# Performance work log

Hardware: AMD Instinct MI355X
Metric: run time of the kernel (lower is better)

The kernel has to match this reference:

```python
import jax, jax.numpy as jnp
import numpy as np
import math

EMBD_SIZE = 1024
OUT_SIZE = 1024
B, N = 8, 2048

def setup_inputs() -> dict:
    key = jax.random.key(0)
    k1, k2, k3 = jax.random.split(key, 3)
    embd = jax.random.normal(k1, (B, N, EMBD_SIZE), dtype=jnp.float32)
    # nn.Linear(embd_size, out_size): weight [out, in], bias [out]
    bound = 1.0 / math.sqrt(EMBD_SIZE)
    W = jax.random.uniform(k2, (OUT_SIZE, EMBD_SIZE), dtype=jnp.float32, minval=-bound, maxval=bound)
    b = jax.random.uniform(k3, (OUT_SIZE,), dtype=jnp.float32, minval=-bound, maxval=bound)
    return {"embd": embd, "W": W, "b": b}

def reference(embd, W, b):
    # c = Linear(embd): [B, N, out_size]
    c = jnp.einsum('bne,oe->bno', embd, W) + b
    # scores = c @ c^T / sqrt(embd_size), softmax over last dim
    score = jnp.einsum('bno,bmo->bnm', c, c) / jnp.sqrt(jnp.float32(EMBD_SIZE))
    score = jax.nn.softmax(score, axis=-1)
    # output = score @ c : [B, N, out_size]
    return jnp.einsum('bnm,bmo->bno', score, c)
```

## Files before the change

### kernel.cpp

```cpp
#include <hip/hip_runtime.h>

typedef unsigned short u16;
typedef unsigned int u32;
typedef __attribute__((ext_vector_type(8))) short short8;
typedef __attribute__((ext_vector_type(4))) float f32x4;

__device__ inline u16 f2bf(float f) {
  u32 x = __float_as_uint(f);
  x += 0x7fff + ((x >> 16) & 1);
  return (u16)(x >> 16);
}
__device__ inline float bf2f(u16 h) {
  return __uint_as_float(((u32)h) << 16);
}
__device__ inline void gload16(const void* g, void* l) {
  __builtin_amdgcn_global_load_lds((const __attribute__((address_space(1))) u32*)g,
                                   (__attribute__((address_space(3))) u32*)l, 16, 0, 0);
}

__device__ inline int sg(int r) {
  return ((r >> 3) & 7) ^ (((r >> 2) & 1) << 2) ^ (((r >> 3) & 1) << 1);
}
__device__ inline int stile_off(int rl, int cl) {
  return rl * 128 + (((cl >> 3) ^ sg(rl)) << 3) + (cl & 7);
}

__global__ void cast_all(const float* __restrict__ embd, const float* __restrict__ W,
                         u16* __restrict__ embd_b, u16* __restrict__ W_b) {
  const float* src; u16* dst; size_t i;
  if (blockIdx.x < 16384) {
    src = embd; dst = embd_b;
    i = ((size_t)blockIdx.x * 256 + threadIdx.x) * 4;
  } else {
    src = W; dst = W_b;
    i = ((size_t)(blockIdx.x - 16384) * 256 + threadIdx.x) * 4;
  }
  float4 v = *(const float4*)(src + i);
  ushort4 o;
  o.x = f2bf(v.x); o.y = f2bf(v.y); o.z = f2bf(v.z); o.w = f2bf(v.w);
  *(ushort4*)(dst + i) = o;
}

#define BM 128
#define BN 128
#define BK 64

template<int MODE>
__global__ __launch_bounds__(256, 2)
void gemm_nt(const u16* __restrict__ A, const u16* __restrict__ B,
             float* __restrict__ Cf, u16* __restrict__ Cb, u16* __restrict__ CT,
             const float* __restrict__ bias, float* __restrict__ rowsum,
             int M, int N, int K, float scale, long sA, long sB, long sC)
{
  __shared__ __align__(16) char smem[32768];
  u16* As = (u16*)smem;
  u16* Bs = As + BM * BK;
  u16* stile = (u16*)smem;

  int z, mBase, nBase, bi = 0, bj = 0;
  if (MODE == 0) {
    z = 0;
    mBase = blockIdx.y * BM;
    nBase = blockIdx.x * BN;
  } else {
    z = blockIdx.x;
    int t = blockIdx.y, row = 0;
    const int nb = N >> 7;
    while (t >= nb - row) { t -= nb - row; ++row; }
    bi = row; bj = row + t;
    mBase = bi * BM; nBase = bj * BN;
  }

  A += (size_t)z * sA;
  B += (size_t)z * sB;
  Cb += (size_t)z * sC;
  if (MODE != 0) rowsum += (size_t)z * M;

  const int tid  = threadIdx.x;
  const int lane = tid & 63;
  const int wave = tid >> 6;
  const int wm = (wave >> 1) * 64;
  const int wn = (wave & 1) * 64;
  const int q = lane >> 4;
  const int r = lane & 15;
  const int rswz = r & 7;

  const int srow = tid >> 3;
  const int scol = ((tid & 7) ^ (srow & 7)) * 8;
  const int lds0 = tid * 16;

  const u16* a0 = A + (size_t)(mBase + srow) * K + scol;
  const u16* b0 = B + (size_t)(nBase + srow) * K + scol;

  f32x4 acc[4][4] = {};

  for (int k0 = 0; k0 < K; k0 += BK) {
#pragma unroll
    for (int i = 0; i < 4; ++i)
      gload16(a0 + (size_t)(32 * i) * K + k0, (char*)As + lds0 + i * 4096);
#pragma unroll
    for (int i = 0; i < 4; ++i)
      gload16(b0 + (size_t)(32 * i) * K + k0, (char*)Bs + lds0 + i * 4096);
    __syncthreads();

#pragma unroll
    for (int kk = 0; kk < 2; ++kk) {
      short8 af[4], bfr[4];
#pragma unroll
      for (int t = 0; t < 4; ++t) {
        const int go = (((kk * 4 + q) ^ rswz)) * 8;
        af[t]  = *(const short8*)(As + (wm + t * 16 + r) * BK + go);
        bfr[t] = *(const short8*)(Bs + (wn + t * 16 + r) * BK + go);
      }
#pragma unroll
      for (int mi = 0; mi < 4; ++mi)
#pragma unroll
        for (int ni = 0; ni < 4; ++ni)
          acc[mi][ni] = __builtin_amdgcn_mfma_f32_16x16x32_bf16(af[mi], bfr[ni], acc[mi][ni], 0, 0, 0);
    }
    __syncthreads();
  }


  if (MODE == 0) {
    float bv[4];
#pragma unroll
    for (int ni = 0; ni < 4; ++ni) bv[ni] = bias[nBase + wn + ni * 16 + r];
#pragma unroll
    for (int mi = 0; mi < 4; ++mi)
#pragma unroll
      for (int ni = 0; ni < 4; ++ni)
#pragma unroll
        for (int reg = 0; reg < 4; ++reg) {
          int rl = wm + mi * 16 + q * 4 + reg;
          int cl = wn + ni * 16 + r;
          stile[stile_off(rl, cl)] = f2bf(acc[mi][ni][reg] + bv[ni]);
        }
    __syncthreads();
    {
      const int z1 = mBase >> 11;
      const int n0 = mBase & 2047;
      u16* ctb = CT + (size_t)z1 * 1024 * 2048;
#pragma unroll
      for (int rnd = 0; rnd < 8; ++rnd) {
        int idx = rnd * 256 + tid;
        int ch = idx & 15, n = idx >> 4;
        short8 v = *(const short8*)(stile + n * 128 + ((ch ^ sg(n)) << 3));
        *(short8*)(Cb + (size_t)(mBase + n) * N + nBase + ch * 8) = v;
      }
#pragma unroll
      for (int rnd = 0; rnd < 8; ++rnd) {
        int idx = rnd * 256 + tid;
        int ch = idx & 15, cc = idx >> 4;
        short8 v;
#pragma unroll
        for (int j = 0; j < 8; ++j) v[j] = (short)stile[stile_off(ch * 8 + j, cc)];
        *(short8*)(ctb + (size_t)(nBase + cc) * 2048 + n0 + ch * 8) = v;
      }
    }
  } else {
    const bool mirror = (bi != bj);
    float colacc[4] = {0.f, 0.f, 0.f, 0.f};
#pragma unroll
    for (int mi = 0; mi < 4; ++mi) {
      float rs[4] = {0.f, 0.f, 0.f, 0.f};
#pragma unroll
      for (int ni = 0; ni < 4; ++ni)
#pragma unroll
        for (int reg = 0; reg < 4; ++reg) {
          float e = __expf(acc[mi][ni][reg] * scale);
          u16 h = f2bf(e);
          float f = bf2f(h);
          rs[reg] += f;
          if (mirror) colacc[ni] += f;
          stile[stile_off(wm + mi * 16 + q * 4 + reg, wn + ni * 16 + r)] = h;
        }
#pragma unroll
      for (int reg = 0; reg < 4; ++reg) {
        float v = rs[reg];
        v += __shfl_xor(v, 1);
        v += __shfl_xor(v, 2);
        v += __shfl_xor(v, 4);
        v += __shfl_xor(v, 8);
        if (r == 0)
          atomicAdd(&rowsum[mBase + wm + mi * 16 + q * 4 + reg], v);
      }
    }
    if (mirror) {
#pragma unroll
      for (int ni = 0; ni < 4; ++ni) {
        float v = colacc[ni];
        v += __shfl_xor(v, 16);
        v += __shfl_xor(v, 32);
        if (q == 0)
          atomicAdd(&rowsum[nBase + wn + ni * 16 + r], v);
      }
    }
    __syncthreads();
#pragma unroll
    for (int rnd = 0; rnd < 8; ++rnd) {
      int idx = rnd * 256 + tid;
      int ch = idx & 15, n = idx >> 4;
      short8 v = *(const short8*)(stile + n * 128 + ((ch ^ sg(n)) << 3));
      *(short8*)(Cb + (size_t)(mBase + n) * N + nBase + ch * 8) = v;
    }
    if (mirror) {
#pragma unroll
      for (int rnd = 0; rnd < 8; ++rnd) {
        int idx = rnd * 256 + tid;
        int ch = idx & 15, cc = idx >> 4;
        short8 v;
#pragma unroll
        for (int j = 0; j < 8; ++j) v[j] = (short)stile[stile_off(ch * 8 + j, cc)];
        *(short8*)(Cb + (size_t)(nBase + cc) * N + mBase + ch * 8) = v;
      }
    }
  }
}

#define STAGE_PV(buf, t) do {                                          \
    const u16* _a = a0 + (size_t)(t) * 64;                             \
    const u16* _b = b0 + (size_t)(t) * 64;                             \
    char* _l = (char*)ldsm + (buf) * 65536 + tid * 16;                 \
    gload16(_a,                      _l);                              \
    gload16(_a +  64 * (size_t)K,    _l + 8192);                       \
    gload16(_a + 128 * (size_t)K,    _l + 16384);                      \
    gload16(_a + 192 * (size_t)K,    _l + 24576);                      \
    gload16(_b,                      _l + 32768);                      \
    gload16(_b +  64 * (size_t)K,    _l + 40960);                      \
    gload16(_b + 128 * (size_t)K,    _l + 49152);                      \
    gload16(_b + 192 * (size_t)K,    _l + 57344);                      \
  } while (0)

__global__ __launch_bounds__(512, 2)
void gemm_pv8(const u16* __restrict__ A, const u16* __restrict__ B,
              float* __restrict__ Cf, const float* __restrict__ rowsum,
              int K, int Nn, long sA, long sB, long sC, int Mrs)
{
  __shared__ __align__(16) u16 ldsm[65536];

  const int z = blockIdx.x;
  const int y = blockIdx.y;
  const int mBase = (y >> 2) * 256;
  const int nBase = (y & 3) * 256;

  A += (size_t)z * sA;
  B += (size_t)z * sB;
  Cf += (size_t)z * sC;
  rowsum += (size_t)z * Mrs;

  const int tid  = threadIdx.x;
  const int lane = tid & 63;
  const int wave = tid >> 6;
  const int wm = (wave >> 2) * 128;
  const int wn = (wave & 3) * 64;
  const int q = lane >> 4;
  const int r = lane & 15;
  const int rx = r & 7;

  const int srow = tid >> 3;
  const int sg8  = ((tid & 7) ^ (srow & 7)) * 8;
  const u16* a0 = A + (size_t)(mBase + srow) * K + sg8;
  const u16* b0 = B + (size_t)(nBase + srow) * K + sg8;

  const int NT = K >> 6;
  const int rA = (wm + r) * 64;
  const int rB = (wn + r) * 64;

  f32x4 acc[8][4] = {};

  STAGE_PV(0, 0);
  STAGE_PV(1, 1);
  asm volatile("s_waitcnt vmcnt(8)" ::: "memory");
  __builtin_amdgcn_s_barrier();

  for (int i = 0; i < NT; ++i) {
    const int d = i & 1;
    const u16* Ab = ldsm + d * 32768;
    const u16* Bb = Ab + 16384;

#pragma unroll
    for (int kk = 0; kk < 2; ++kk) {
      const int gq = ((kk * 4 + q) ^ rx) * 8;
      short8 bfr[4];
#pragma unroll
      for (int t = 0; t < 4; ++t)
        bfr[t] = *(const short8*)(Bb + rB + t * 1024 + gq);
#pragma unroll
      for (int mh = 0; mh < 2; ++mh) {
        short8 af[4];
#pragma unroll
        for (int t = 0; t < 4; ++t)
          af[t] = *(const short8*)(Ab + rA + (mh * 4 + t) * 1024 + gq);
        __builtin_amdgcn_s_setprio(1);
#pragma unroll
        for (int mi = 0; mi < 4; ++mi)
#pragma unroll
          for (int ni = 0; ni < 4; ++ni)
            acc[mh * 4 + mi][ni] = __builtin_amdgcn_mfma_f32_16x16x32_bf16(
                af[mi], bfr[ni], acc[mh * 4 + mi][ni], 0, 0, 0);
        __builtin_amdgcn_s_setprio(0);
      }
    }

    __builtin_amdgcn_s_barrier();
    if (i + 2 < NT) {
      STAGE_PV(d, i + 2);
      asm volatile("s_waitcnt vmcnt(8)" ::: "memory");
    } else {
      asm volatile("s_waitcnt vmcnt(0)" ::: "memory");
    }
    __builtin_amdgcn_s_barrier();
    __builtin_amdgcn_sched_barrier(0);
  }

#pragma unroll
  for (int mi = 0; mi < 8; ++mi)
#pragma unroll
    for (int reg = 0; reg < 4; ++reg) {
      const int row = mBase + wm + mi * 16 + q * 4 + reg;
      const float inv = 1.0f / rowsum[row];
      float* crow = Cf + (size_t)row * Nn + nBase + wn + r;
#pragma unroll
      for (int ni = 0; ni < 4; ++ni)
        crow[ni * 16] = acc[mi][ni][reg] * inv;
    }
}

extern "C" void kernel_launch(void* const* d_in, const int* in_sizes, int n_in,
                              void* d_out, int out_size, void* d_ws, size_t ws_size,
                              hipStream_t stream) {
  const float* embd = (const float*)d_in[0];
  const float* W    = (const float*)d_in[1];
  const float* bias = (const float*)d_in[2];
  float* out = (float*)d_out;

  char* ws = (char*)d_ws;
  u16* P_b    = (u16*)(ws + 0);
  u16* embd_b = (u16*)(ws + 0);
  u16* W_b    = (u16*)(ws + 33554432);
  u16* c_b    = (u16*)(ws + 67108864);
  u16* cT_b   = (u16*)(ws + 100663296);
  float* rowsum = (float*)(ws + 134217728);

  cast_all<<<17408, 256, 0, stream>>>(embd, W, embd_b, W_b);

  gemm_nt<0><<<dim3(8, 128, 1), 256, 0, stream>>>(
      embd_b, W_b, nullptr, c_b, cT_b, bias, nullptr,
      16384, 1024, 1024, 0.f, 0, 0, 0);

  hipMemsetAsync(rowsum, 0, 16384 * sizeof(float), stream);

  gemm_nt<1><<<dim3(8, 136, 1), 256, 0, stream>>>(
      c_b, c_b, nullptr, P_b, nullptr, nullptr, rowsum,
      2048, 2048, 1024, 0.03125f, 2048L * 1024, 2048L * 1024, 2048L * 2048);

  gemm_pv8<<<dim3(8, 32, 1), 512, 0, stream>>>(
      P_b, cT_b, out, rowsum,
      2048, 1024, 2048L * 2048, 2048L * 1024, 2048L * 1024, 2048);
}
```

Measured before the change: 289.8 us.

## Restructure PV GEMM into 4-stage K=32 pipeline with split A/B staging

The P·V GEMM kernel now uses K-tiles of 32 instead of 64 and a four-buffer LDS ring with three tiles in flight, where the previous version used double buffering. Global-to-LDS loads for A and B are issued separately, interleaved between the two halves of the MFMA work, with barriers placed so loads overlap compute. The goal is to hide global memory latency better and smooth LDS traffic, at the cost of more barriers per unit of K and a changed swizzle that must stay bank-conflict free.

```diff
diff --git a/kernel.cpp b/kernel.cpp
--- a/kernel.cpp
+++ b/kernel.cpp
@@ -218,18 +218,17 @@
   }
 }
 
-#define STAGE_PV(buf, t) do {                                          \
-    const u16* _a = a0 + (size_t)(t) * 64;                             \
-    const u16* _b = b0 + (size_t)(t) * 64;                             \
-    char* _l = (char*)ldsm + (buf) * 65536 + tid * 16;                 \
-    gload16(_a,                      _l);                              \
-    gload16(_a +  64 * (size_t)K,    _l + 8192);                       \
-    gload16(_a + 128 * (size_t)K,    _l + 16384);                      \
-    gload16(_a + 192 * (size_t)K,    _l + 24576);                      \
-    gload16(_b,                      _l + 32768);                      \
-    gload16(_b +  64 * (size_t)K,    _l + 40960);                      \
-    gload16(_b + 128 * (size_t)K,    _l + 49152);                      \
-    gload16(_b + 192 * (size_t)K,    _l + 57344);                      \
+#define PV_STAGE_A(f, t) do {                                           \
+    const u16* _a = a0 + (size_t)(t) * 32;                              \
+    char* _l = (char*)ldsm + (f) * 32768 + tid * 16;                    \
+    gload16(_a, _l);                                                    \
+    gload16(_a + 128 * (size_t)K, _l + 8192);                           \
+  } while (0)
+#define PV_STAGE_B(f, t) do {                                           \
+    const u16* _b = b0 + (size_t)(t) * 32;                              \
+    char* _l = (char*)ldsm + (f) * 32768 + 16384 + tid * 16;            \
+    gload16(_b, _l);                                                    \
+    gload16(_b + 128 * (size_t)K, _l + 8192);                           \
   } while (0)
 
 __global__ __launch_bounds__(512, 2)
@@ -256,62 +255,69 @@
   const int wn = (wave & 3) * 64;
   const int q = lane >> 4;
   const int r = lane & 15;
-  const int rx = r & 7;
-
-  const int srow = tid >> 3;
-  const int sg8  = ((tid & 7) ^ (srow & 7)) * 8;
-  const u16* a0 = A + (size_t)(mBase + srow) * K + sg8;
-  const u16* b0 = B + (size_t)(nBase + srow) * K + sg8;
-
-  const int NT = K >> 6;
-  const int rA = (wm + r) * 64;
-  const int rB = (wn + r) * 64;
+  const int gq = ((q ^ (r & 3)) << 3);
+
+  const int srow = tid >> 2;
+  const int sgr  = ((tid & 3) ^ (srow & 3)) * 8;
+  const u16* a0 = A + (size_t)(mBase + srow) * K + sgr;
+  const u16* b0 = B + (size_t)(nBase + srow) * K + sgr;
+
+  const int NT = K >> 5;
+  const int rA = (wm + r) * 32;
+  const int rB = (wn + r) * 32;
 
   f32x4 acc[8][4] = {};
 
-  STAGE_PV(0, 0);
-  STAGE_PV(1, 1);
+  PV_STAGE_A(0, 0); PV_STAGE_B(0, 0);
+  PV_STAGE_A(1, 1); PV_STAGE_B(1, 1);
+  PV_STAGE_A(2, 2); PV_STAGE_B(2, 2);
   asm volatile("s_waitcnt vmcnt(8)" ::: "memory");
   __builtin_amdgcn_s_barrier();
 
   for (int i = 0; i < NT; ++i) {
-    const int d = i & 1;
-    const u16* Ab = ldsm + d * 32768;
-    const u16* Bb = Ab + 16384;
-
-#pragma unroll
-    for (int kk = 0; kk < 2; ++kk) {
-      const int gq = ((kk * 4 + q) ^ rx) * 8;
-      short8 bfr[4];
-#pragma unroll
-      for (int t = 0; t < 4; ++t)
-        bfr[t] = *(const short8*)(Bb + rB + t * 1024 + gq);
-#pragma unroll
-      for (int mh = 0; mh < 2; ++mh) {
-        short8 af[4];
-#pragma unroll
-        for (int t = 0; t < 4; ++t)
-          af[t] = *(const short8*)(Ab + rA + (mh * 4 + t) * 1024 + gq);
-        __builtin_amdgcn_s_setprio(1);
-#pragma unroll
-        for (int mi = 0; mi < 4; ++mi)
-#pragma unroll
-          for (int ni = 0; ni < 4; ++ni)
-            acc[mh * 4 + mi][ni] = __builtin_amdgcn_mfma_f32_16x16x32_bf16(
-                af[mi], bfr[ni], acc[mh * 4 + mi][ni], 0, 0, 0);
-        __builtin_amdgcn_s_setprio(0);
-      }
-    }
-
-    __builtin_amdgcn_s_barrier();
-    if (i + 2 < NT) {
-      STAGE_PV(d, i + 2);
-      asm volatile("s_waitcnt vmcnt(8)" ::: "memory");
-    } else {
-      asm volatile("s_waitcnt vmcnt(0)" ::: "memory");
-    }
+    __builtin_amdgcn_sched_barrier(0);
+    const u16* Ab = ldsm + (i & 3) * 16384;
+    const u16* Bb = Ab + 8192;
+    const int f = (i + 3) & 3;
+
+    short8 bfr[4], af[4];
+#pragma unroll
+    for (int t = 0; t < 4; ++t)
+      bfr[t] = *(const short8*)(Bb + rB + t * 512 + gq);
+#pragma unroll
+    for (int t = 0; t < 4; ++t)
+      af[t] = *(const short8*)(Ab + rA + t * 512 + gq);
+    if (i + 3 < NT) PV_STAGE_A(f, i + 3);
     __builtin_amdgcn_s_barrier();
     __builtin_amdgcn_sched_barrier(0);
+    __builtin_amdgcn_s_setprio(1);
+#pragma unroll
+    for (int mi = 0; mi < 4; ++mi)
+#pragma unroll
+      for (int ni = 0; ni < 4; ++ni)
+        acc[mi][ni] = __builtin_amdgcn_mfma_f32_16x16x32_bf16(
+            af[mi], bfr[ni], acc[mi][ni], 0, 0, 0);
+    __builtin_amdgcn_s_setprio(0);
+    __builtin_amdgcn_s_barrier();
+
+#pragma unroll
+    for (int t = 0; t < 4; ++t)
+      af[t] = *(const short8*)(Ab + rA + 2048 + t * 512 + gq);
+    if (i + 3 < NT) PV_STAGE_B(f, i + 3);
+    if (i + 3 < NT)      asm volatile("s_waitcnt vmcnt(8)" ::: "memory");
+    else if (i + 2 < NT) asm volatile("s_waitcnt vmcnt(4)" ::: "memory");
+    else                 asm volatile("s_waitcnt vmcnt(0)" ::: "memory");
+    __builtin_amdgcn_s_barrier();
+    __builtin_amdgcn_sched_barrier(0);
+    __builtin_amdgcn_s_setprio(1);
+#pragma unroll
+    for (int mi = 0; mi < 4; ++mi)
+#pragma unroll
+      for (int ni = 0; ni < 4; ++ni)
+        acc[4 + mi][ni] = __builtin_amdgcn_mfma_f32_16x16x32_bf16(
+            af[mi], bfr[ni], acc[4 + mi][ni], 0, 0, 0);
+    __builtin_amdgcn_s_setprio(0);
+    __builtin_amdgcn_s_barrier();
   }
 
 #pragma unroll
```

Result: slower. 302.4 us (+4.3%).
